# Performance work log

Measured on AMD Instinct MI355X. Metric: run time of the kernel, lower is better.

## Reference

```python
import jax, jax.numpy as jnp
import numpy as np

VDD = 1.8
NBITS = 4
VR = VDD / 2 ** NBITS   # LSB voltage
VREF = VR
DELTA = 1e-30
LENGTH = 500000
NADC = 24               # 2 * p * number_of_samples = 2*3*4
NW = NBITS * (NBITS + 1) // 2  # 10 weights consumed by the SAR recurrence


def setup_inputs() -> dict:
    key = jax.random.key(0)
    k1, k2 = jax.random.split(key)
    x = jax.random.uniform(k1, (LENGTH, NADC), dtype=jnp.float32)
    W = jax.random.uniform(k2, (NW,), dtype=jnp.float32)
    return {"x": x, "W": W}


def reference(x, W):
    # Bit-serial SAR-ADC successive approximation. NBITS is small and the
    # weight index m is statically unrolled exactly as in the torch loop.
    Qs = [None] * NBITS  # Qs[j] : [length, nadc] sign of bit j
    m = NW - 1
    for j in reversed(range(NBITS)):
        bit_sum = W[m] * VREF
        m -= 1
        for k in range(j + 1, NBITS):
            bit_sum = bit_sum + (Qs[k] + 1.0) * 0.5 * W[m] * VR
            m -= 1
        Qs[j] = jnp.sign(x - bit_sum + DELTA)
    Q = jnp.stack(Qs, axis=-1)  # [length, nadc, nbits]
    bit_weights = (VR * (2.0 ** jnp.arange(NBITS))).astype(x.dtype)  # [nbits]
    q = jnp.sum((Q + 1.0) * 0.5 * bit_weights, axis=-1)  # [length, nadc]
    return q.astype(jnp.float32), Q.astype(jnp.float32)
```

## Files before the change

kernel.cpp:

```cpp
#include <hip/hip_runtime.h>


__global__ __launch_bounds__(256)
void sar_adc_kernel(const float* __restrict__ x, const float* __restrict__ W,
                    float* __restrict__ q_out, float4* __restrict__ Q4, int n)
{
    const int tid  = threadIdx.x;
    const int base = blockIdx.x * 1024 + tid;

    const float VREF = 0.1125f;
    const float VR   = 0.1125f;

    float w0 = W[0], w1 = W[1], w2 = W[2], w3 = W[3], w4 = W[4];
    float w5 = W[5], w6 = W[6], w7 = W[7], w8 = W[8], w9 = W[9];

    float wv0 = __fmul_rn(w0, VR);
    float wv1 = __fmul_rn(w1, VR);
    float wv2 = __fmul_rn(w2, VR);
    float wv4 = __fmul_rn(w4, VR);
    float wv5 = __fmul_rn(w5, VR);
    float wv7 = __fmul_rn(w7, VR);

    float b3     = __fmul_rn(w9, VREF);
    float b2base = __fmul_rn(w8, VREF);
    float b1base = __fmul_rn(w6, VREF);
    float b0base = __fmul_rn(w3, VREF);

    float xe[4];
    #pragma unroll
    for (int j = 0; j < 4; ++j) {
        int e = base + j * 256;
        if (e < n) xe[j] = x[e];
    }

    const float bw0 = 0.1125f, bw1 = 0.225f, bw2 = 0.45f, bw3 = 0.9f;

    #pragma unroll
    for (int j = 0; j < 4; ++j) {
        int e = base + j * 256;
        if (e >= n) continue;
        float xv = xe[j];

        bool s3 = (xv >= b3);

        float b2 = b2base;
        if (s3) b2 = __fadd_rn(b2, wv7);
        bool s2 = (xv >= b2);

        float b1 = b1base;
        if (s2) b1 = __fadd_rn(b1, wv5);
        if (s3) b1 = __fadd_rn(b1, wv4);
        bool s1 = (xv >= b1);

        float b0 = b0base;
        if (s1) b0 = __fadd_rn(b0, wv2);
        if (s2) b0 = __fadd_rn(b0, wv1);
        if (s3) b0 = __fadd_rn(b0, wv0);
        bool s0 = (xv >= b0);

        float qv = s0 ? bw0 : 0.0f;
        if (s1) qv = __fadd_rn(qv, bw1);
        if (s2) qv = __fadd_rn(qv, bw2);
        if (s3) qv = __fadd_rn(qv, bw3);
        q_out[e] = qv;

        float4 Qv;
        Qv.x = s0 ? 1.0f : -1.0f;
        Qv.y = s1 ? 1.0f : -1.0f;
        Qv.z = s2 ? 1.0f : -1.0f;
        Qv.w = s3 ? 1.0f : -1.0f;
        Q4[e] = Qv;
    }
}

extern "C" void kernel_launch(void* const* d_in, const int* in_sizes, int n_in,
                              void* d_out, int out_size, void* d_ws, size_t ws_size,
                              hipStream_t stream)
{
    const float* x = (const float*)d_in[0];
    const float* W = (const float*)d_in[1];
    int n = in_sizes[0];

    float* q  = (float*)d_out;
    float4* Q = (float4*)((float*)d_out + n);

    const int block = 256;
    const int per_block = 1024;
    const int grid = (n + per_block - 1) / per_block;
    sar_adc_kernel<<<grid, block, 0, stream>>>(x, W, q, Q, n);
}
```

Baseline: 270.9 us.

## Vectorize x/q accesses as float4 and stage Q writes through swizzled LDS

Each thread now loads four contiguous x values as one float4 and writes its four q results as one float4, instead of strided scalar accesses. The per-element Q float4 outputs are staged in a swizzled shared-memory buffer and written back after a barrier so that consecutive threads store consecutive Q entries. The aim is fewer, wider global memory transactions on a bandwidth-bound kernel. It adds a __syncthreads and LDS traffic. It also assumes n is a multiple of 4 and that the x and q pointers are 16-byte aligned.

New measurement: 271.6 us. Within noise of the previous version (+0.3%).

```diff
diff --git a/kernel.cpp b/kernel.cpp
--- a/kernel.cpp
+++ b/kernel.cpp
@@ -2,11 +2,14 @@
 
 
 __global__ __launch_bounds__(256)
-void sar_adc_kernel(const float* __restrict__ x, const float* __restrict__ W,
-                    float* __restrict__ q_out, float4* __restrict__ Q4, int n)
+void sar_adc_kernel(const float4* __restrict__ x4, const float* __restrict__ W,
+                    float4* __restrict__ q4, float4* __restrict__ Q4, int n)
 {
-    const int tid  = threadIdx.x;
-    const int base = blockIdx.x * 1024 + tid;
+    __shared__ float4 lds[1024];
+
+    const int tid = threadIdx.x;
+    const int e0  = blockIdx.x * 1024;
+    const int t4  = blockIdx.x * 256 + tid;
 
     const float VREF = 0.1125f;
     const float VR   = 0.1125f;
@@ -26,50 +29,61 @@
     float b1base = __fmul_rn(w6, VREF);
     float b0base = __fmul_rn(w3, VREF);
 
-    float xe[4];
-    #pragma unroll
-    for (int j = 0; j < 4; ++j) {
-        int e = base + j * 256;
-        if (e < n) xe[j] = x[e];
-    }
+    const bool in = (4 * t4 < n);
+    float4 xv = make_float4(0.f, 0.f, 0.f, 0.f);
+    if (in) xv = x4[t4];
 
     const float bw0 = 0.1125f, bw1 = 0.225f, bw2 = 0.45f, bw3 = 0.9f;
 
+    float xe[4] = {xv.x, xv.y, xv.z, xv.w};
+    float qe[4];
+
     #pragma unroll
     for (int j = 0; j < 4; ++j) {
-        int e = base + j * 256;
-        if (e >= n) continue;
-        float xv = xe[j];
+        float xj = xe[j];
 
-        bool s3 = (xv >= b3);
+        bool s3 = (xj >= b3);
 
         float b2 = b2base;
         if (s3) b2 = __fadd_rn(b2, wv7);
-        bool s2 = (xv >= b2);
+        bool s2 = (xj >= b2);
 
         float b1 = b1base;
         if (s2) b1 = __fadd_rn(b1, wv5);
         if (s3) b1 = __fadd_rn(b1, wv4);
-        bool s1 = (xv >= b1);
+        bool s1 = (xj >= b1);
 
         float b0 = b0base;
         if (s1) b0 = __fadd_rn(b0, wv2);
         if (s2) b0 = __fadd_rn(b0, wv1);
         if (s3) b0 = __fadd_rn(b0, wv0);
-        bool s0 = (xv >= b0);
+        bool s0 = (xj >= b0);
 
         float qv = s0 ? bw0 : 0.0f;
         if (s1) qv = __fadd_rn(qv, bw1);
         if (s2) qv = __fadd_rn(qv, bw2);
         if (s3) qv = __fadd_rn(qv, bw3);
-        q_out[e] = qv;
+        qe[j] = qv;
 
         float4 Qv;
         Qv.x = s0 ? 1.0f : -1.0f;
         Qv.y = s1 ? 1.0f : -1.0f;
         Qv.z = s2 ? 1.0f : -1.0f;
         Qv.w = s3 ? 1.0f : -1.0f;
-        Q4[e] = Qv;
+        int s = 4 * tid + j;
+        lds[s ^ ((s >> 4) & 3)] = Qv;
+    }
+
+    if (in) q4[t4] = make_float4(qe[0], qe[1], qe[2], qe[3]);
+
+    __syncthreads();
+
+    #pragma unroll
+    for (int p = 0; p < 4; ++p) {
+        int s = tid + 256 * p;
+        float4 v = lds[s ^ ((s >> 4) & 3)];
+        int g = e0 + s;
+        if (g < n) Q4[g] = v;
     }
 }
 
@@ -87,5 +101,6 @@
     const int block = 256;
     const int per_block = 1024;
     const int grid = (n + per_block - 1) / per_block;
-    sar_adc_kernel<<<grid, block, 0, stream>>>(x, W, q, Q, n);
+    sar_adc_kernel<<<grid, block, 0, stream>>>(
+        (const float4*)x, W, (float4*)q, Q, n);
 }
```
